# Performance work log

Measured on AMD Instinct MI355X. Metric: run time of the kernel, lower is better.

Reference implementation:

```python
import jax, jax.numpy as jnp
import numpy as np

INV_SQRT_4PI = 0.28209479177387814  # 1/sqrt(4*pi)

def sh_l(r, l):
    """Real spherical harmonics of unit vectors r [..., 3], e3nn order,
    'integral' normalization (e3nn o3.spherical_harmonics default)."""
    x, y, z = r[..., 0], r[..., 1], r[..., 2]
    if l == 0:
        return jnp.full(r.shape[:-1] + (1,), INV_SQRT_4PI, r.dtype)
    if l == 1:
        return 0.4886025119029199 * r  # sqrt(3/(4pi)) * (x, y, z)
    s15 = 3.872983346207417 * INV_SQRT_4PI   # sqrt(15)/sqrt(4pi)
    s5 = 2.23606797749979 * INV_SQRT_4PI     # sqrt(5)/sqrt(4pi)
    return jnp.stack([
        s15 * x * z,
        s15 * x * y,
        s5 * (y * y - 0.5 * (x * x + z * z)),
        s15 * y * z,
        0.5 * s15 * (z * z - x * x),
    ], axis=-1)

def layer_norm(x, g, b, eps=1e-5):
    mu = jnp.mean(x, axis=-1, keepdims=True)
    var = jnp.mean((x - mu) ** 2, axis=-1, keepdims=True)
    return (x - mu) * jax.lax.rsqrt(var + eps) * g + b

def setup_inputs() -> dict:
    key = jax.random.key(0)
    N, C, L = 1024, 128, 3  # nodes, sphere_channels, lmax+1
    ks = jax.random.split(key, 12)
    s = 0.02
    return {
        "x_emb": jax.random.normal(ks[0], (N, 9, C), jnp.float32),
        "pos": jax.random.normal(ks[1], (N, 3), jnp.float32) * 3.0,
        "q_w": jax.random.normal(ks[2], (C, C), jnp.float32) * s,
        "q_b": jnp.zeros((C,), jnp.float32),
        "k_w": jax.random.normal(ks[3], (C, C), jnp.float32) * s,
        "k_b": jnp.zeros((C,), jnp.float32),
        "v_w": jax.random.normal(ks[4], (L, C, C), jnp.float32) * s,
        "v_b0": jnp.zeros((C,), jnp.float32),
        "out_w": jax.random.normal(ks[5], (L, C, C), jnp.float32) * s,
        "ln_g": jnp.ones((L, C), jnp.float32),
        "ln_b": jnp.zeros((L, C), jnp.float32),
        "batch": jnp.sort(jax.random.randint(ks[6], (N,), 0, 16)).astype(jnp.int64),
    }

def reference(x_emb, pos, q_w, q_b, k_w, k_b, v_w, v_b0, out_w, ln_g, ln_b, batch):
    N, _, C = x_emb.shape
    H = 8
    D = C // H
    degs = (1, 3, 5)  # 2l+1 for l = 0, 1, 2

    # pairwise unit displacements  [N, N, 3]
    diff = pos[:, None, :] - pos[None, :, :]
    dist = jnp.maximum(jnp.linalg.norm(diff, axis=-1, keepdims=True), 1e-8)
    r_hat = diff / dist

    same = batch[:, None] == batch[None, :]           # [N, N]
    valid = same & ~jnp.eye(N, dtype=bool)

    # per-degree features: split x_emb[:, 9, C] into [1, 3, 5]
    feats = [x_emb[:, 0:1], x_emb[:, 1:4], x_emb[:, 4:9]]

    # HTR invariant pairwise score  [N, N, C]
    score = jnp.zeros((N, N, C), x_emb.dtype)
    for l, f in enumerate(feats):
        sh = sh_l(r_hat, l)                           # [N, N, 2l+1]
        score = score + jnp.einsum('imc,ijm->ijc', f, sh) / degs[l]
    score = score * valid[..., None].astype(score.dtype)

    q = (score.mean(axis=1) @ q_w.T + q_b).reshape(N, H, D)
    k = (score.mean(axis=0) @ k_w.T + k_b).reshape(N, H, D)

    attn = jnp.einsum('ihd,jhd->hij', q, k) * (D ** -0.5)
    attn = jnp.where(same[None], attn, -jnp.inf)
    attn = jnp.nan_to_num(jax.nn.softmax(attn, axis=-1))

    outs = []
    for l, f in enumerate(feats):
        m = degs[l]
        v = f @ v_w[l].T
        if l == 0:
            v = v + v_b0
        v = v.reshape(N, m, H, D)
        o = jnp.einsum('hij,jmhd->imhd', attn, v).reshape(N, m, C)
        o = o @ out_w[l].T
        outs.append(layer_norm(f + o, ln_g[l], ln_b[l]))
    return jnp.concatenate(outs, axis=1)
```

## Files before the change

### kernel.cpp

```cpp
#include <hip/hip_runtime.h>
#include <hip/hip_bf16.h>
#include <math.h>

#define NN 1024

typedef __attribute__((ext_vector_type(8))) short bf16x8;
typedef __attribute__((ext_vector_type(4))) float f32x4;

__device__ __forceinline__ float wave_sum(float v) {
#pragma unroll
  for (int off = 32; off > 0; off >>= 1) v += __shfl_down(v, off);
  return v;
}
__device__ __forceinline__ float wave_max(float v) {
#pragma unroll
  for (int off = 32; off > 0; off >>= 1) v = fmaxf(v, __shfl_down(v, off));
  return v;
}
__device__ __forceinline__ short f2bf(float x) {
  __hip_bfloat16 b = __float2bfloat16(x);
  return *(short*)&b;
}

#define SH_C0 0.28209479177387814f
#define SH_C1 0.4886025119029199f
#define SH_S15 1.0925484305920792f
#define SH_S5 0.6307831305050401f

__global__ __launch_bounds__(256) void htr_geom(
    const float* __restrict__ qw, const float* __restrict__ kw,
    const float* __restrict__ vw, const float* __restrict__ ow,
    const float* __restrict__ x_emb, const float* __restrict__ pos,
    const int* __restrict__ batch, short* __restrict__ wbf,
    short* __restrict__ x_bf, short* __restrict__ fT,
    short* __restrict__ Wsh, short* __restrict__ rowm_bf) {
  const int b = blockIdx.x;
  const int tid = threadIdx.x;
  __shared__ short tile[128][34];
  __shared__ float red[4][9];
  __shared__ float sm[9];

  if (b < 8) {
    const float* src;
    if (b == 0) src = qw;
    else if (b == 1) src = kw;
    else if (b < 5) src = vw + (b - 2) * 16384;
    else src = ow + (b - 5) * 16384;
    short* dst = wbf + b * 16384;
    for (int idx = tid; idx < 16384; idx += 256) dst[idx] = f2bf(src[idx]);
  } else if (b < 1160) {
    int base = (b - 8) * 1024 + tid * 4;
    float4 v = *(const float4*)(x_emb + base);
    *(short4*)(x_bf + base) = make_short4(f2bf(v.x), f2bf(v.y), f2bf(v.z), f2bf(v.w));
  } else if (b < 1448) {
    const int sub = b - 1160;
    const int i0 = (sub & 31) * 32;
    const int m = sub >> 5;
#pragma unroll
    for (int it = 0; it < 16; ++it) {
      int e = tid + it * 256;
      int r = e >> 7, c = e & 127;
      tile[c][r] = f2bf(x_emb[((i0 + r) * 9 + m) * 128 + c]);
    }
    __syncthreads();
#pragma unroll
    for (int it = 0; it < 8; ++it) {
      int idx = tid + it * 256;
      int c = idx >> 4, ii2 = idx & 15;
      *(short2*)(fT + c * 9216 + m * 1024 + i0 + ii2 * 2) =
          make_short2(tile[c][ii2 * 2], tile[c][ii2 * 2 + 1]);
    }
  } else if (b < 2472) {
    const int j = b - 1448;
    const float pjx = pos[j * 3 + 0], pjy = pos[j * 3 + 1], pjz = pos[j * 3 + 2];
    const int bj = batch[j];
    short* wrow = Wsh + j * 9216;
    for (int i = tid; i < 1024; i += 256) {
      float dx = pos[i * 3 + 0] - pjx;
      float dy = pos[i * 3 + 1] - pjy;
      float dz = pos[i * 3 + 2] - pjz;
      bool ok = (i != j) && (batch[i] == bj);
      float okf = ok ? 1.f : 0.f;
      float d2 = dx * dx + dy * dy + dz * dz;
      float inv = okf / fmaxf(sqrtf(d2), 1e-8f);
      float x = dx * inv, y = dy * inv, z = dz * inv;
      wrow[0 * 1024 + i] = f2bf(SH_C0 * okf);
      wrow[1 * 1024 + i] = f2bf((SH_C1 * (1.f / 3.f)) * x);
      wrow[2 * 1024 + i] = f2bf((SH_C1 * (1.f / 3.f)) * y);
      wrow[3 * 1024 + i] = f2bf((SH_C1 * (1.f / 3.f)) * z);
      wrow[4 * 1024 + i] = f2bf((SH_S15 * 0.2f) * x * z);
      wrow[5 * 1024 + i] = f2bf((SH_S15 * 0.2f) * x * y);
      wrow[6 * 1024 + i] = f2bf((SH_S5 * 0.2f) * (y * y - 0.5f * (x * x + z * z)));
      wrow[7 * 1024 + i] = f2bf((SH_S15 * 0.2f) * y * z);
      wrow[8 * 1024 + i] = f2bf((0.5f * SH_S15 * 0.2f) * (z * z - x * x));
    }
  } else {
    const int i = b - 2472;
    const float px = pos[i * 3 + 0], py = pos[i * 3 + 1], pz = pos[i * 3 + 2];
    const int bi = batch[i];
    float s[9];
#pragma unroll
    for (int m = 0; m < 9; ++m) s[m] = 0.f;
    for (int j = tid; j < NN; j += 256) {
      if (j == i) continue;
      if (batch[j] != bi) continue;
      float dx = px - pos[j * 3 + 0];
      float dy = py - pos[j * 3 + 1];
      float dz = pz - pos[j * 3 + 2];
      float d2 = dx * dx + dy * dy + dz * dz;
      float inv = 1.0f / fmaxf(sqrtf(d2), 1e-8f);
      float x = dx * inv, y = dy * inv, z = dz * inv;
      s[0] += 1.0f;
      s[1] += x; s[2] += y; s[3] += z;
      s[4] += x * z; s[5] += x * y;
      s[6] += y * y - 0.5f * (x * x + z * z);
      s[7] += y * z;
      s[8] += z * z - x * x;
    }
    const int wave = tid >> 6, lane = tid & 63;
#pragma unroll
    for (int m = 0; m < 9; ++m) {
      float v = wave_sum(s[m]);
      if (lane == 0) red[wave][m] = v;
    }
    __syncthreads();
    if (tid < 9) {
      float v = red[0][tid] + red[1][tid] + red[2][tid] + red[3][tid];
      float scl = SH_S15 * 0.2f;
      if (tid == 0) scl = SH_C0;
      else if (tid < 4) scl = SH_C1 * (1.f / 3.f);
      else if (tid == 6) scl = SH_S5 * 0.2f;
      else if (tid == 8) scl = 0.5f * SH_S15 * 0.2f;
      sm[tid] = v * scl * (1.0f / 1024.0f);
    }
    __syncthreads();
    if (tid < 128) {
      float acc = 0.f;
#pragma unroll
      for (int m = 0; m < 9; ++m)
        acc = fmaf(sm[m], x_emb[(i * 9 + m) * 128 + tid], acc);
      rowm_bf[i * 128 + tid] = f2bf(acc);
    }
  }
}

#define CMS 16
__global__ __launch_bounds__(64) void htr_colmean_mfma(
    const short* __restrict__ Wsh, const short* __restrict__ fT,
    float* __restrict__ part) {
  const int jbase = blockIdx.x * 16;
  const int ks = blockIdx.y;
  const int lane = threadIdx.x;
  const int q = lane >> 4, l15 = lane & 15;
  const short* ap = Wsh + (jbase + l15) * 9216 + ks * 576 + q * 8;
  const short* bp = fT + l15 * 9216 + ks * 576 + q * 8;
  f32x4 acc[8];
#pragma unroll
  for (int t = 0; t < 8; ++t) acc[t] = (f32x4){0.f, 0.f, 0.f, 0.f};
  bf16x8 a = *(const bf16x8*)ap;
  bf16x8 b[8];
#pragma unroll
  for (int t = 0; t < 8; ++t) b[t] = *(const bf16x8*)(bp + t * 147456);
  for (int s = 1; s < 18; ++s) {
    const int off = s * 32;
    bf16x8 an = *(const bf16x8*)(ap + off);
    bf16x8 bn[8];
#pragma unroll
    for (int t = 0; t < 8; ++t) bn[t] = *(const bf16x8*)(bp + t * 147456 + off);
#pragma unroll
    for (int t = 0; t < 8; ++t)
      acc[t] = __builtin_amdgcn_mfma_f32_16x16x32_bf16(a, b[t], acc[t], 0, 0, 0);
    a = an;
#pragma unroll
    for (int t = 0; t < 8; ++t) b[t] = bn[t];
  }
#pragma unroll
  for (int t = 0; t < 8; ++t)
    acc[t] = __builtin_amdgcn_mfma_f32_16x16x32_bf16(a, b[t], acc[t], 0, 0, 0);
#pragma unroll
  for (int t = 0; t < 8; ++t)
#pragma unroll
    for (int r = 0; r < 4; ++r)
      part[(ks * 1024 + jbase + q * 4 + r) * 128 + t * 16 + l15] = acc[t][r];
}

__global__ __launch_bounds__(64) void htr_proj(
    const short* __restrict__ rowm_bf, const float* __restrict__ part,
    const short* __restrict__ x_bf, const short* __restrict__ wbf,
    const float* __restrict__ q_b, const float* __restrict__ k_b,
    const float* __restrict__ v_b0, float* __restrict__ qbuf,
    float* __restrict__ khbuf, short* __restrict__ vbT) {
  const int ibase = blockIdx.x * 16;
  const int y = blockIdx.y;
  const int lane = threadIdx.x;
  const int q = lane >> 4, l15 = lane & 15;

  bf16x8 a[4];
  const short* bp;
  if (y == 0) {
    const short* ap = rowm_bf + (ibase + l15) * 128 + q * 8;
#pragma unroll
    for (int ks = 0; ks < 4; ++ks) a[ks] = *(const bf16x8*)(ap + ks * 32);
    bp = wbf + l15 * 128 + q * 8;
  } else if (y == 1) {
    const float* pp = part + (size_t)(ibase + l15) * 128;
#pragma unroll
    for (int ks = 0; ks < 4; ++ks) {
      float s0 = 0.f, s1 = 0.f, s2 = 0.f, s3 = 0.f;
      float s4 = 0.f, s5 = 0.f, s6 = 0.f, s7 = 0.f;
#pragma unroll
      for (int s = 0; s < CMS; ++s) {
        const float* ps = pp + s * 131072 + ks * 32 + q * 8;
        float4 u0 = *(const float4*)(ps);
        float4 u1 = *(const float4*)(ps + 4);
        s0 += u0.x; s1 += u0.y; s2 += u0.z; s3 += u0.w;
        s4 += u1.x; s5 += u1.y; s6 += u1.z; s7 += u1.w;
      }
      const float sc = 1.0f / 1024.0f;
      bf16x8 av;
      av[0] = f2bf(s0 * sc); av[1] = f2bf(s1 * sc);
      av[2] = f2bf(s2 * sc); av[3] = f2bf(s3 * sc);
      av[4] = f2bf(s4 * sc); av[5] = f2bf(s5 * sc);
      av[6] = f2bf(s6 * sc); av[7] = f2bf(s7 * sc);
      a[ks] = av;
    }
    bp = wbf + 16384 + l15 * 128 + q * 8;
  } else {
    const int m = y - 2;
    const int l = (m == 0) ? 0 : ((m < 4) ? 1 : 2);
    const short* ap = x_bf + ((ibase + l15) * 9 + m) * 128 + q * 8;
#pragma unroll
    for (int ks = 0; ks < 4; ++ks) a[ks] = *(const bf16x8*)(ap + ks * 32);
    bp = wbf + (2 + l) * 16384 + l15 * 128 + q * 8;
  }

  f32x4 acc[8];
#pragma unroll
  for (int t = 0; t < 8; ++t) {
    acc[t] = (f32x4){0.f, 0.f, 0.f, 0.f};
    const short* bt = bp + t * 2048;
#pragma unroll
    for (int ks = 0; ks < 4; ++ks) {
      bf16x8 b = *(const bf16x8*)(bt + ks * 32);
      acc[t] = __builtin_amdgcn_mfma_f32_16x16x32_bf16(a[ks], b, acc[t], 0, 0, 0);
    }
  }

  if (y == 0) {
#pragma unroll
    for (int t = 0; t < 8; ++t) {
      float bo = q_b[t * 16 + l15];
#pragma unroll
      for (int r = 0; r < 4; ++r)
        qbuf[(ibase + q * 4 + r) * 128 + t * 16 + l15] = acc[t][r] + bo;
    }
  } else if (y == 1) {
#pragma unroll
    for (int t = 0; t < 8; ++t) {
      float bo = k_b[t * 16 + l15];
#pragma unroll
      for (int r = 0; r < 4; ++r)
        khbuf[(t * 1024 + ibase + q * 4 + r) * 16 + l15] = acc[t][r] + bo;
    }
  } else {
    const int m = y - 2;
#pragma unroll
    for (int t = 0; t < 8; ++t) {
      float bias = (m == 0) ? v_b0[t * 16 + l15] : 0.f;
#pragma unroll
      for (int r = 0; r < 4; ++r)
        vbT[(t * 144 + m * 16 + l15) * 1024 + ibase + q * 4 + r] =
            f2bf(acc[t][r] + bias);
    }
  }
}

__global__ __launch_bounds__(256) void htr_attn8(
    const float* __restrict__ qbuf, const float* __restrict__ khbuf,
    const int* __restrict__ batch, short* __restrict__ attn) {
  const int ibase = blockIdx.x * 8;
  const int h = blockIdx.y;
  const int tid = threadIdx.x;
  const int g = tid >> 7;
  const int lj = tid & 127;
  const int i0 = ibase + g * 4;
  float qr[4][16];
  int bi[4];
#pragma unroll
  for (int r = 0; r < 4; ++r) {
    bi[r] = batch[i0 + r];
#pragma unroll
    for (int d = 0; d < 16; ++d)
      qr[r][d] = qbuf[(i0 + r) * 128 + h * 16 + d] * 0.25f;
  }
  float s[4][8];
#pragma unroll
  for (int jt = 0; jt < 8; ++jt) {
    int j = jt * 128 + lj;
    int bj = batch[j];
    const float4* kp = (const float4*)(khbuf + (h * 1024 + j) * 16);
    float4 k0 = kp[0], k1 = kp[1], k2 = kp[2], k3 = kp[3];
#pragma unroll
    for (int r = 0; r < 4; ++r) {
      float d = 0.f;
      d = fmaf(qr[r][0], k0.x, d);  d = fmaf(qr[r][1], k0.y, d);
      d = fmaf(qr[r][2], k0.z, d);  d = fmaf(qr[r][3], k0.w, d);
      d = fmaf(qr[r][4], k1.x, d);  d = fmaf(qr[r][5], k1.y, d);
      d = fmaf(qr[r][6], k1.z, d);  d = fmaf(qr[r][7], k1.w, d);
      d = fmaf(qr[r][8], k2.x, d);  d = fmaf(qr[r][9], k2.y, d);
      d = fmaf(qr[r][10], k2.z, d); d = fmaf(qr[r][11], k2.w, d);
      d = fmaf(qr[r][12], k3.x, d); d = fmaf(qr[r][13], k3.y, d);
      d = fmaf(qr[r][14], k3.z, d); d = fmaf(qr[r][15], k3.w, d);
      s[r][jt] = (bj == bi[r]) ? d : -INFINITY;
    }
  }
  const int wig = (tid >> 6) & 1, lane = tid & 63;
  __shared__ float redm[2][4][2], reds[2][4][2];
#pragma unroll
  for (int r = 0; r < 4; ++r) {
    float mx = s[r][0];
#pragma unroll
    for (int jt = 1; jt < 8; ++jt) mx = fmaxf(mx, s[r][jt]);
    mx = wave_max(mx);
    if (lane == 0) redm[g][r][wig] = mx;
  }
  __syncthreads();
  float M[4];
#pragma unroll
  for (int r = 0; r < 4; ++r) M[r] = fmaxf(redm[g][r][0], redm[g][r][1]);
#pragma unroll
  for (int r = 0; r < 4; ++r) {
    float t = 0.f;
#pragma unroll
    for (int jt = 0; jt < 8; ++jt) {
      s[r][jt] = expf(s[r][jt] - M[r]);
      t += s[r][jt];
    }
    t = wave_sum(t);
    if (lane == 0) reds[g][r][wig] = t;
  }
  __syncthreads();
#pragma unroll
  for (int r = 0; r < 4; ++r) {
    float inv = 1.0f / (reds[g][r][0] + reds[g][r][1]);
    short* dp = attn + (h * 1024 + i0 + r) * 1024;
#pragma unroll
    for (int jt = 0; jt < 8; ++jt) dp[jt * 128 + lj] = f2bf(s[r][jt] * inv);
  }
}

template <int NT0, int NT>
__device__ __forceinline__ void apply_body(
    const short* __restrict__ attn, const short* __restrict__ vbT,
    short* __restrict__ obuf_bf, int ibase, int h, int lane) {
  const int q = lane >> 4, l15 = lane & 15;
  const short* ap = attn + (h * 1024 + ibase + l15) * 1024 + q * 8;
  const short* bp = vbT + (h * 144 + l15) * 1024 + q * 8;
  f32x4 acc[NT];
#pragma unroll
  for (int t = 0; t < NT; ++t) acc[t] = (f32x4){0.f, 0.f, 0.f, 0.f};
  bf16x8 a = *(const bf16x8*)ap;
  bf16x8 b[NT];
#pragma unroll
  for (int t = 0; t < NT; ++t) b[t] = *(const bf16x8*)(bp + (NT0 + t) * 16384);
  for (int ks = 1; ks < 32; ++ks) {
    const int off = ks * 32;
    bf16x8 an = *(const bf16x8*)(ap + off);
    bf16x8 bn[NT];
#pragma unroll
    for (int t = 0; t < NT; ++t)
      bn[t] = *(const bf16x8*)(bp + (NT0 + t) * 16384 + off);
#pragma unroll
    for (int t = 0; t < NT; ++t)
      acc[t] = __builtin_amdgcn_mfma_f32_16x16x32_bf16(a, b[t], acc[t], 0, 0, 0);
    a = an;
#pragma unroll
    for (int t = 0; t < NT; ++t) b[t] = bn[t];
  }
#pragma unroll
  for (int t = 0; t < NT; ++t)
    acc[t] = __builtin_amdgcn_mfma_f32_16x16x32_bf16(a, b[t], acc[t], 0, 0, 0);
#pragma unroll
  for (int t = 0; t < NT; ++t)
#pragma unroll
    for (int r = 0; r < 4; ++r)
      obuf_bf[((ibase + q * 4 + r) * 9 + NT0 + t) * 128 + h * 16 + l15] =
          f2bf(acc[t][r]);
}

__global__ __launch_bounds__(64) void htr_apply_mfma(
    const short* __restrict__ attn, const short* __restrict__ vbT,
    short* __restrict__ obuf_bf) {
  const int ibase = blockIdx.x * 16;
  const int h = blockIdx.y;
  if (blockIdx.z == 0)
    apply_body<0, 5>(attn, vbT, obuf_bf, ibase, h, threadIdx.x);
  else
    apply_body<5, 4>(attn, vbT, obuf_bf, ibase, h, threadIdx.x);
}

__global__ __launch_bounds__(64) void htr_outln_mfma(
    const short* __restrict__ obuf_bf, const float* __restrict__ x_emb,
    const short* __restrict__ wbf, const float* __restrict__ ln_g,
    const float* __restrict__ ln_b, float* __restrict__ out) {
  const int ibase = blockIdx.x * 16;
  const int m = blockIdx.y;
  const int l = (m == 0) ? 0 : ((m < 4) ? 1 : 2);
  const int lane = threadIdx.x;
  const int q = lane >> 4, l15 = lane & 15;
  const short* ap = obuf_bf + ((ibase + l15) * 9 + m) * 128 + q * 8;
  const short* bp = wbf + (5 + l) * 16384 + l15 * 128 + q * 8;
  bf16x8 a[4];
#pragma unroll
  for (int ks = 0; ks < 4; ++ks) a[ks] = *(const bf16x8*)(ap + ks * 32);
  f32x4 acc[8];
#pragma unroll
  for (int t = 0; t < 8; ++t) {
    acc[t] = (f32x4){0.f, 0.f, 0.f, 0.f};
    const short* bt = bp + t * 2048;
#pragma unroll
    for (int ks = 0; ks < 4; ++ks) {
      bf16x8 b = *(const bf16x8*)(bt + ks * 32);
      acc[t] = __builtin_amdgcn_mfma_f32_16x16x32_bf16(a[ks], b, acc[t], 0, 0, 0);
    }
  }
  float g[8], bb[8];
#pragma unroll
  for (int t = 0; t < 8; ++t) {
    g[t] = ln_g[l * 128 + t * 16 + l15];
    bb[t] = ln_b[l * 128 + t * 16 + l15];
  }
#pragma unroll
  for (int r = 0; r < 4; ++r) {
    const int i = ibase + q * 4 + r;
    const float* xr = x_emb + (i * 9 + m) * 128;
    float v[8];
    float sv = 0.f, sq = 0.f;
#pragma unroll
    for (int t = 0; t < 8; ++t) {
      v[t] = acc[t][r] + xr[t * 16 + l15];
      sv += v[t];
      sq += v[t] * v[t];
    }
#pragma unroll
    for (int off = 1; off < 16; off <<= 1) {
      sv += __shfl_xor(sv, off);
      sq += __shfl_xor(sq, off);
    }
    float mu = sv * (1.f / 128.f);
    float var = sq * (1.f / 128.f) - mu * mu;
    float rs = rsqrtf(var + 1e-5f);
    float* orow = out + (i * 9 + m) * 128;
#pragma unroll
    for (int t = 0; t < 8; ++t)
      orow[t * 16 + l15] = (v[t] - mu) * rs * g[t] + bb[t];
  }
}

extern "C" void kernel_launch(void* const* d_in, const int* in_sizes, int n_in,
                              void* d_out, int out_size, void* d_ws, size_t ws_size,
                              hipStream_t stream) {
  (void)in_sizes; (void)n_in; (void)out_size; (void)ws_size;
  const float* x_emb = (const float*)d_in[0];
  const float* pos   = (const float*)d_in[1];
  const float* q_w   = (const float*)d_in[2];
  const float* q_b   = (const float*)d_in[3];
  const float* k_w   = (const float*)d_in[4];
  const float* k_b   = (const float*)d_in[5];
  const float* v_w   = (const float*)d_in[6];
  const float* v_b0  = (const float*)d_in[7];
  const float* out_w = (const float*)d_in[8];
  const float* ln_g  = (const float*)d_in[9];
  const float* ln_b  = (const float*)d_in[10];
  const int*   batch = (const int*)d_in[11];
  float* out = (float*)d_out;

  float* ws = (float*)d_ws;
  short* rowm_bf = (short*)(ws + 0);
  float* qbuf    = ws + 65536;
  float* khbuf   = ws + 196608;
  short* wbf     = (short*)(ws + 327680);
  short* x_bf    = (short*)(ws + 393216);
  short* vbT     = (short*)(ws + 983040);
  short* obuf_bf = (short*)(ws + 1572864);
  short* attn    = (short*)(ws + 2162688);
  float* part    = ws + 2162688;
  short* Wsh     = (short*)(ws + 6356992);
  short* fT      = (short*)(ws + 11075584);

  htr_geom<<<3496, 256, 0, stream>>>(q_w, k_w, v_w, out_w, x_emb, pos, batch,
                                     wbf, x_bf, fT, Wsh, rowm_bf);
  htr_colmean_mfma<<<dim3(64, CMS), 64, 0, stream>>>(Wsh, fT, part);
  htr_proj<<<dim3(64, 11), 64, 0, stream>>>(rowm_bf, part, x_bf, wbf, q_b, k_b,
                                            v_b0, qbuf, khbuf, vbT);
  htr_attn8<<<dim3(128, 8), 256, 0, stream>>>(qbuf, khbuf, batch, attn);
  htr_apply_mfma<<<dim3(64, 8, 2), 64, 0, stream>>>(attn, vbT, obuf_bf);
  htr_outln_mfma<<<dim3(64, 9), 64, 0, stream>>>(obuf_bf, x_emb, wbf, ln_g,
                                                 ln_b, out);
}
```

Before: 172.9 us.

## Fuse attention softmax and value apply into one MFMA flash kernel

```diff
diff --git a/kernel.cpp b/kernel.cpp
--- a/kernel.cpp
+++ b/kernel.cpp
@@ -10,11 +10,6 @@
 __device__ __forceinline__ float wave_sum(float v) {
 #pragma unroll
   for (int off = 32; off > 0; off >>= 1) v += __shfl_down(v, off);
-  return v;
-}
-__device__ __forceinline__ float wave_max(float v) {
-#pragma unroll
-  for (int off = 32; off > 0; off >>= 1) v = fmaxf(v, __shfl_down(v, off));
   return v;
 }
 __device__ __forceinline__ short f2bf(float x) {
@@ -144,7 +139,7 @@
   }
 }
 
-#define CMS 16
+#define CMS 32
 __global__ __launch_bounds__(64) void htr_colmean_mfma(
     const short* __restrict__ Wsh, const short* __restrict__ fT,
     float* __restrict__ part) {
@@ -152,8 +147,8 @@
   const int ks = blockIdx.y;
   const int lane = threadIdx.x;
   const int q = lane >> 4, l15 = lane & 15;
-  const short* ap = Wsh + (jbase + l15) * 9216 + ks * 576 + q * 8;
-  const short* bp = fT + l15 * 9216 + ks * 576 + q * 8;
+  const short* ap = Wsh + (jbase + l15) * 9216 + ks * 288 + q * 8;
+  const short* bp = fT + l15 * 9216 + ks * 288 + q * 8;
   f32x4 acc[8];
 #pragma unroll
   for (int t = 0; t < 8; ++t) acc[t] = (f32x4){0.f, 0.f, 0.f, 0.f};
@@ -161,7 +156,7 @@
   bf16x8 b[8];
 #pragma unroll
   for (int t = 0; t < 8; ++t) b[t] = *(const bf16x8*)(bp + t * 147456);
-  for (int s = 1; s < 18; ++s) {
+  for (int s = 1; s < 9; ++s) {
     const int off = s * 32;
     bf16x8 an = *(const bf16x8*)(ap + off);
     bf16x8 bn[8];
@@ -188,8 +183,8 @@
     const short* __restrict__ rowm_bf, const float* __restrict__ part,
     const short* __restrict__ x_bf, const short* __restrict__ wbf,
     const float* __restrict__ q_b, const float* __restrict__ k_b,
-    const float* __restrict__ v_b0, float* __restrict__ qbuf,
-    float* __restrict__ khbuf, short* __restrict__ vbT) {
+    const float* __restrict__ v_b0, short* __restrict__ qb16,
+    short* __restrict__ khbT, short* __restrict__ vbT) {
   const int ibase = blockIdx.x * 16;
   const int y = blockIdx.y;
   const int lane = threadIdx.x;
@@ -208,7 +203,6 @@
     for (int ks = 0; ks < 4; ++ks) {
       float s0 = 0.f, s1 = 0.f, s2 = 0.f, s3 = 0.f;
       float s4 = 0.f, s5 = 0.f, s6 = 0.f, s7 = 0.f;
-#pragma unroll
       for (int s = 0; s < CMS; ++s) {
         const float* ps = pp + s * 131072 + ks * 32 + q * 8;
         float4 u0 = *(const float4*)(ps);
@@ -251,16 +245,22 @@
     for (int t = 0; t < 8; ++t) {
       float bo = q_b[t * 16 + l15];
 #pragma unroll
-      for (int r = 0; r < 4; ++r)
-        qbuf[(ibase + q * 4 + r) * 128 + t * 16 + l15] = acc[t][r] + bo;
+      for (int r = 0; r < 4; ++r) {
+        int i = ibase + q * 4 + r;
+        qb16[(t * 1024 + i) * 32 + l15] = f2bf((acc[t][r] + bo) * 0.25f);
+        qb16[(t * 1024 + i) * 32 + 16 + l15] = 0;
+      }
     }
   } else if (y == 1) {
 #pragma unroll
     for (int t = 0; t < 8; ++t) {
       float bo = k_b[t * 16 + l15];
 #pragma unroll
-      for (int r = 0; r < 4; ++r)
-        khbuf[(t * 1024 + ibase + q * 4 + r) * 16 + l15] = acc[t][r] + bo;
+      for (int r = 0; r < 4; ++r) {
+        int j = ibase + q * 4 + r;
+        khbT[(t * 1024 + j) * 32 + l15] = f2bf(acc[t][r] + bo);
+        khbT[(t * 1024 + j) * 32 + 16 + l15] = 0;
+      }
     }
   } else {
     const int m = y - 2;
@@ -275,128 +275,112 @@
   }
 }
 
-__global__ __launch_bounds__(256) void htr_attn8(
-    const float* __restrict__ qbuf, const float* __restrict__ khbuf,
-    const int* __restrict__ batch, short* __restrict__ attn) {
-  const int ibase = blockIdx.x * 8;
-  const int h = blockIdx.y;
-  const int tid = threadIdx.x;
-  const int g = tid >> 7;
-  const int lj = tid & 127;
-  const int i0 = ibase + g * 4;
-  float qr[4][16];
-  int bi[4];
-#pragma unroll
-  for (int r = 0; r < 4; ++r) {
-    bi[r] = batch[i0 + r];
-#pragma unroll
-    for (int d = 0; d < 16; ++d)
-      qr[r][d] = qbuf[(i0 + r) * 128 + h * 16 + d] * 0.25f;
-  }
-  float s[4][8];
-#pragma unroll
-  for (int jt = 0; jt < 8; ++jt) {
-    int j = jt * 128 + lj;
-    int bj = batch[j];
-    const float4* kp = (const float4*)(khbuf + (h * 1024 + j) * 16);
-    float4 k0 = kp[0], k1 = kp[1], k2 = kp[2], k3 = kp[3];
-#pragma unroll
-    for (int r = 0; r < 4; ++r) {
-      float d = 0.f;
-      d = fmaf(qr[r][0], k0.x, d);  d = fmaf(qr[r][1], k0.y, d);
-      d = fmaf(qr[r][2], k0.z, d);  d = fmaf(qr[r][3], k0.w, d);
-      d = fmaf(qr[r][4], k1.x, d);  d = fmaf(qr[r][5], k1.y, d);
-      d = fmaf(qr[r][6], k1.z, d);  d = fmaf(qr[r][7], k1.w, d);
-      d = fmaf(qr[r][8], k2.x, d);  d = fmaf(qr[r][9], k2.y, d);
-      d = fmaf(qr[r][10], k2.z, d); d = fmaf(qr[r][11], k2.w, d);
-      d = fmaf(qr[r][12], k3.x, d); d = fmaf(qr[r][13], k3.y, d);
-      d = fmaf(qr[r][14], k3.z, d); d = fmaf(qr[r][15], k3.w, d);
-      s[r][jt] = (bj == bi[r]) ? d : -INFINITY;
-    }
-  }
-  const int wig = (tid >> 6) & 1, lane = tid & 63;
-  __shared__ float redm[2][4][2], reds[2][4][2];
-#pragma unroll
-  for (int r = 0; r < 4; ++r) {
-    float mx = s[r][0];
-#pragma unroll
-    for (int jt = 1; jt < 8; ++jt) mx = fmaxf(mx, s[r][jt]);
-    mx = wave_max(mx);
-    if (lane == 0) redm[g][r][wig] = mx;
-  }
-  __syncthreads();
-  float M[4];
-#pragma unroll
-  for (int r = 0; r < 4; ++r) M[r] = fmaxf(redm[g][r][0], redm[g][r][1]);
-#pragma unroll
-  for (int r = 0; r < 4; ++r) {
-    float t = 0.f;
-#pragma unroll
-    for (int jt = 0; jt < 8; ++jt) {
-      s[r][jt] = expf(s[r][jt] - M[r]);
-      t += s[r][jt];
-    }
-    t = wave_sum(t);
-    if (lane == 0) reds[g][r][wig] = t;
-  }
-  __syncthreads();
-#pragma unroll
-  for (int r = 0; r < 4; ++r) {
-    float inv = 1.0f / (reds[g][r][0] + reds[g][r][1]);
-    short* dp = attn + (h * 1024 + i0 + r) * 1024;
-#pragma unroll
-    for (int jt = 0; jt < 8; ++jt) dp[jt * 128 + lj] = f2bf(s[r][jt] * inv);
-  }
-}
-
-template <int NT0, int NT>
-__device__ __forceinline__ void apply_body(
-    const short* __restrict__ attn, const short* __restrict__ vbT,
-    short* __restrict__ obuf_bf, int ibase, int h, int lane) {
-  const int q = lane >> 4, l15 = lane & 15;
-  const short* ap = attn + (h * 1024 + ibase + l15) * 1024 + q * 8;
-  const short* bp = vbT + (h * 144 + l15) * 1024 + q * 8;
-  f32x4 acc[NT];
-#pragma unroll
-  for (int t = 0; t < NT; ++t) acc[t] = (f32x4){0.f, 0.f, 0.f, 0.f};
-  bf16x8 a = *(const bf16x8*)ap;
-  bf16x8 b[NT];
-#pragma unroll
-  for (int t = 0; t < NT; ++t) b[t] = *(const bf16x8*)(bp + (NT0 + t) * 16384);
-  for (int ks = 1; ks < 32; ++ks) {
-    const int off = ks * 32;
-    bf16x8 an = *(const bf16x8*)(ap + off);
-    bf16x8 bn[NT];
-#pragma unroll
-    for (int t = 0; t < NT; ++t)
-      bn[t] = *(const bf16x8*)(bp + (NT0 + t) * 16384 + off);
-#pragma unroll
-    for (int t = 0; t < NT; ++t)
-      acc[t] = __builtin_amdgcn_mfma_f32_16x16x32_bf16(a, b[t], acc[t], 0, 0, 0);
-    a = an;
-#pragma unroll
-    for (int t = 0; t < NT; ++t) b[t] = bn[t];
-  }
-#pragma unroll
-  for (int t = 0; t < NT; ++t)
-    acc[t] = __builtin_amdgcn_mfma_f32_16x16x32_bf16(a, b[t], acc[t], 0, 0, 0);
-#pragma unroll
-  for (int t = 0; t < NT; ++t)
-#pragma unroll
-    for (int r = 0; r < 4; ++r)
-      obuf_bf[((ibase + q * 4 + r) * 9 + NT0 + t) * 128 + h * 16 + l15] =
-          f2bf(acc[t][r]);
-}
-
-__global__ __launch_bounds__(64) void htr_apply_mfma(
-    const short* __restrict__ attn, const short* __restrict__ vbT,
+#define PPITCH 1040
+__global__ __launch_bounds__(256) void htr_flash(
+    const short* __restrict__ qb16,
+    const short* __restrict__ khbT,
+    const short* __restrict__ vbT,
+    const int* __restrict__ batch,
     short* __restrict__ obuf_bf) {
   const int ibase = blockIdx.x * 16;
   const int h = blockIdx.y;
-  if (blockIdx.z == 0)
-    apply_body<0, 5>(attn, vbT, obuf_bf, ibase, h, threadIdx.x);
-  else
-    apply_body<5, 4>(attn, vbT, obuf_bf, ibase, h, threadIdx.x);
+  const int tid = threadIdx.x;
+  const int w = tid >> 6;
+  const int lane = tid & 63;
+  const int q = lane >> 4, l15 = lane & 15;
+  __shared__ short P[16][PPITCH];
+  __shared__ int bsh[1024];
+  __shared__ float redM[4][16], redS[4][16];
+
+  for (int idx = tid; idx < 1024; idx += 256) bsh[idx] = batch[idx];
+  __syncthreads();
+  int bi[4];
+#pragma unroll
+  for (int r = 0; r < 4; ++r) bi[r] = bsh[ibase + q * 4 + r];
+
+  bf16x8 aq = *(const bf16x8*)(qb16 + (h * 1024 + ibase + l15) * 32 + q * 8);
+  f32x4 sc[16];
+#pragma unroll
+  for (int jt = 0; jt < 16; ++jt) {
+    int jb = w * 256 + jt * 16;
+    bf16x8 bk = *(const bf16x8*)(khbT + (h * 1024 + jb + l15) * 32 + q * 8);
+    sc[jt] = __builtin_amdgcn_mfma_f32_16x16x32_bf16(
+        aq, bk, (f32x4){0.f, 0.f, 0.f, 0.f}, 0, 0, 0);
+    int bj = bsh[jb + l15];
+#pragma unroll
+    for (int r = 0; r < 4; ++r)
+      if (bj != bi[r]) sc[jt][r] = -INFINITY;
+  }
+  float mx[4];
+#pragma unroll
+  for (int r = 0; r < 4; ++r) {
+    float m = sc[0][r];
+#pragma unroll
+    for (int jt = 1; jt < 16; ++jt) m = fmaxf(m, sc[jt][r]);
+#pragma unroll
+    for (int off = 1; off < 16; off <<= 1) m = fmaxf(m, __shfl_xor(m, off));
+    mx[r] = m;
+  }
+  if (l15 == 0) {
+#pragma unroll
+    for (int r = 0; r < 4; ++r) redM[w][q * 4 + r] = mx[r];
+  }
+  __syncthreads();
+  float M[4];
+#pragma unroll
+  for (int r = 0; r < 4; ++r) {
+    int row = q * 4 + r;
+    M[r] = fmaxf(fmaxf(redM[0][row], redM[1][row]),
+                 fmaxf(redM[2][row], redM[3][row]));
+  }
+  float sm[4] = {0.f, 0.f, 0.f, 0.f};
+#pragma unroll
+  for (int jt = 0; jt < 16; ++jt) {
+#pragma unroll
+    for (int r = 0; r < 4; ++r) {
+      float e = __expf(sc[jt][r] - M[r]);
+      sc[jt][r] = e;
+      sm[r] += e;
+    }
+  }
+#pragma unroll
+  for (int r = 0; r < 4; ++r) {
+#pragma unroll
+    for (int off = 1; off < 16; off <<= 1) sm[r] += __shfl_xor(sm[r], off);
+  }
+  if (l15 == 0) {
+#pragma unroll
+    for (int r = 0; r < 4; ++r) redS[w][q * 4 + r] = sm[r];
+  }
+  __syncthreads();
+  float inv[4];
+#pragma unroll
+  for (int r = 0; r < 4; ++r) {
+    int row = q * 4 + r;
+    inv[r] = 1.0f / (redS[0][row] + redS[1][row] + redS[2][row] + redS[3][row]);
+  }
+#pragma unroll
+  for (int jt = 0; jt < 16; ++jt) {
+    int col = w * 256 + jt * 16 + l15;
+#pragma unroll
+    for (int r = 0; r < 4; ++r)
+      P[q * 4 + r][col] = f2bf(sc[jt][r] * inv[r]);
+  }
+  __syncthreads();
+  for (int t = w; t < 9; t += 4) {
+    f32x4 o = (f32x4){0.f, 0.f, 0.f, 0.f};
+    const short* apv = vbT + (h * 144 + t * 16 + l15) * 1024 + q * 8;
+#pragma unroll
+    for (int kc = 0; kc < 32; ++kc) {
+      bf16x8 av = *(const bf16x8*)(apv + kc * 32);
+      bf16x8 bv = *(const bf16x8*)(&P[l15][kc * 32 + q * 8]);
+      o = __builtin_amdgcn_mfma_f32_16x16x32_bf16(av, bv, o, 0, 0, 0);
+    }
+#pragma unroll
+    for (int r = 0; r < 4; ++r)
+      obuf_bf[((ibase + l15) * 9 + t) * 128 + h * 16 + q * 4 + r] =
+          f2bf(o[r]);
+  }
 }
 
 __global__ __launch_bounds__(64) void htr_outln_mfma(
@@ -477,13 +461,12 @@
 
   float* ws = (float*)d_ws;
   short* rowm_bf = (short*)(ws + 0);
-  float* qbuf    = ws + 65536;
-  float* khbuf   = ws + 196608;
+  short* qb16    = (short*)(ws + 65536);
+  short* khbT    = (short*)(ws + 196608);
   short* wbf     = (short*)(ws + 327680);
   short* x_bf    = (short*)(ws + 393216);
   short* vbT     = (short*)(ws + 983040);
   short* obuf_bf = (short*)(ws + 1572864);
-  short* attn    = (short*)(ws + 2162688);
   float* part    = ws + 2162688;
   short* Wsh     = (short*)(ws + 6356992);
   short* fT      = (short*)(ws + 11075584);
@@ -492,9 +475,8 @@
                                      wbf, x_bf, fT, Wsh, rowm_bf);
   htr_colmean_mfma<<<dim3(64, CMS), 64, 0, stream>>>(Wsh, fT, part);
   htr_proj<<<dim3(64, 11), 64, 0, stream>>>(rowm_bf, part, x_bf, wbf, q_b, k_b,
-                                            v_b0, qbuf, khbuf, vbT);
-  htr_attn8<<<dim3(128, 8), 256, 0, stream>>>(qbuf, khbuf, batch, attn);
-  htr_apply_mfma<<<dim3(64, 8, 2), 64, 0, stream>>>(attn, vbT, obuf_bf);
+                                            v_b0, qb16, khbT, vbT);
+  htr_flash<<<dim3(64, 8), 256, 0, stream>>>(qb16, khbT, vbT, batch, obuf_bf);
   htr_outln_mfma<<<dim3(64, 9), 64, 0, stream>>>(obuf_bf, x_emb, wbf, ln_g,
                                                  ln_b, out);
 }
```

Result: slower. 178.7 us (+3.4%).
